# Optimization experiments

Measured on AMD Instinct MI355X. Metric: run time of the kernel, lower is better.

Reference implementation:

```python
import jax, jax.numpy as jnp
import numpy as np

NHEAD, D_K, D_V, D_MODEL = 16, 64, 64, 1024
B, LQ, LK = 2, 2048, 2048
LN_EPS = 1e-6


def setup_inputs() -> dict:
    key = jax.random.key(0)
    ks = jax.random.split(key, 12)
    s = 0.02
    return {
        "q": jax.random.normal(ks[0], (B, LQ, D_MODEL), jnp.float32),
        "k": jax.random.normal(ks[1], (B, LK, D_MODEL), jnp.float32),
        "v": jax.random.normal(ks[2], (B, LK, D_MODEL), jnp.float32),
        "mask": jax.random.randint(ks[3], (B, LQ, LK), 0, 2, jnp.int32),
        "mean": jax.random.uniform(ks[4], (B, LK), jnp.float32, 0.5, 1.5),
        "std": jax.random.uniform(ks[5], (B, LK), jnp.float32, -0.5, 0.5),
        "w_qs": jax.random.normal(ks[6], (D_MODEL, NHEAD * D_K), jnp.float32) * s,
        "w_ks": jax.random.normal(ks[7], (D_MODEL, NHEAD * D_K), jnp.float32) * s,
        "w_vs": jax.random.normal(ks[8], (D_MODEL, NHEAD * D_V), jnp.float32) * s,
        "w_fc": jax.random.normal(ks[9], (NHEAD * D_V, D_MODEL), jnp.float32) * s,
        "ln_gamma": jnp.ones((D_MODEL,), jnp.float32),
        "ln_beta": jnp.zeros((D_MODEL,), jnp.float32),
    }


def _layer_norm(x, gamma, beta):
    mu = jnp.mean(x, axis=-1, keepdims=True)
    var = jnp.mean(jnp.square(x - mu), axis=-1, keepdims=True)
    return (x - mu) * jax.lax.rsqrt(var + LN_EPS) * gamma + beta


def reference(q, k, v, mask, mean, std, w_qs, w_ks, w_vs, w_fc, ln_gamma, ln_beta):
    residual = q
    # projections -> [B, H, L, d]
    qh = (q @ w_qs).reshape(B, LQ, NHEAD, D_K).transpose(0, 2, 1, 3)
    kh = (k @ w_ks).reshape(B, LK, NHEAD, D_K).transpose(0, 2, 1, 3)
    vh = (v @ w_vs).reshape(B, LK, NHEAD, D_V).transpose(0, 2, 1, 3)
    # scores with affine modification: (QK^T * mean + std) / sqrt(d_k)
    attn = jnp.einsum("bhqd,bhkd->bhqk", qh, kh)
    attn = (attn * mean[:, None, None, :] + std[:, None, None, :]) / jnp.sqrt(jnp.float32(D_K))
    attn = jnp.where(mask[:, None, :, :] == 0, jnp.float32(-1e9), attn)
    attn = jax.nn.softmax(attn, axis=-1)
    out = jnp.einsum("bhqk,bhkd->bhqd", attn, vh)  # [B,H,Lq,Dv]
    out = out.transpose(0, 2, 1, 3).reshape(B, LQ, NHEAD * D_V)
    out = out @ w_fc + residual
    return _layer_norm(out, ln_gamma, ln_beta)
```

## Files before the change

kernel.cpp:

```cpp
#include <hip/hip_runtime.h>
#include <math.h>

#define NHEAD 16
#define DK 64
#define DMODEL 1024
#define BB 2
#define LQ 2048
#define LK 2048
#define MROWS (BB * LQ)

typedef __attribute__((ext_vector_type(8))) short short8v;
typedef __attribute__((ext_vector_type(4))) float f32x4;
typedef __attribute__((ext_vector_type(16))) float f32x16;

__device__ __forceinline__ ushort f2bf(float x) {
  uint u = __builtin_bit_cast(uint, x);
  u += 0x7FFFu + ((u >> 16) & 1u);
  return (ushort)(u >> 16);
}
__device__ __forceinline__ float bf2f(ushort h) {
  return __builtin_bit_cast(float, ((uint)h) << 16);
}

__global__ __launch_bounds__(256) void conv_x(const float* __restrict__ x,
                                              ushort* __restrict__ hi,
                                              ushort* __restrict__ lo, int n4) {
  for (int i = blockIdx.x * blockDim.x + threadIdx.x; i < n4;
       i += gridDim.x * blockDim.x) {
    float4 v = ((const float4*)x)[i];
    ushort4 h, l;
    h.x = f2bf(v.x); l.x = f2bf(v.x - bf2f(h.x));
    h.y = f2bf(v.y); l.y = f2bf(v.y - bf2f(h.y));
    h.z = f2bf(v.z); l.z = f2bf(v.z - bf2f(h.z));
    h.w = f2bf(v.w); l.w = f2bf(v.w - bf2f(h.w));
    ((ushort4*)hi)[i] = h;
    ((ushort4*)lo)[i] = l;
  }
}

__global__ __launch_bounds__(256) void conv_wT(
    const float* __restrict__ w0, const float* __restrict__ w1,
    const float* __restrict__ w2, const float* __restrict__ w3,
    ushort* __restrict__ hiB, ushort* __restrict__ loB) {
  const float* W = blockIdx.z == 0 ? w0
                   : blockIdx.z == 1 ? w1
                   : blockIdx.z == 2 ? w2 : w3;
  ushort* hi = hiB + (size_t)blockIdx.z * DMODEL * DMODEL;
  ushort* lo = loB + (size_t)blockIdx.z * DMODEL * DMODEL;
  __shared__ ushort Th[64][66], Tl[64][66];
  const int t = threadIdx.x;
  const int n0 = blockIdx.x * 64, k0 = blockIdx.y * 64;
  const int r = t >> 4, c4 = (t & 15) << 2;
#pragma unroll
  for (int p = 0; p < 4; ++p) {
    const int kr = r + p * 16;
    float4 v = *(const float4*)&W[(size_t)(k0 + kr) * DMODEL + n0 + c4];
    ushort h;
    h = f2bf(v.x); Th[c4 + 0][kr] = h; Tl[c4 + 0][kr] = f2bf(v.x - bf2f(h));
    h = f2bf(v.y); Th[c4 + 1][kr] = h; Tl[c4 + 1][kr] = f2bf(v.y - bf2f(h));
    h = f2bf(v.z); Th[c4 + 2][kr] = h; Tl[c4 + 2][kr] = f2bf(v.z - bf2f(h));
    h = f2bf(v.w); Th[c4 + 3][kr] = h; Tl[c4 + 3][kr] = f2bf(v.w - bf2f(h));
  }
  __syncthreads();
  const int n = t >> 2, g = t & 3;
  uint uh[8], ul[8];
#pragma unroll
  for (int j = 0; j < 8; ++j) {
    uh[j] = *(const uint*)&Th[n][g * 16 + 2 * j];
    ul[j] = *(const uint*)&Tl[n][g * 16 + 2 * j];
  }
  const size_t ob = (size_t)(n0 + n) * DMODEL + k0 + g * 16;
  *(uint4*)&hi[ob] = make_uint4(uh[0], uh[1], uh[2], uh[3]);
  *(uint4*)&hi[ob + 8] = make_uint4(uh[4], uh[5], uh[6], uh[7]);
  *(uint4*)&lo[ob] = make_uint4(ul[0], ul[1], ul[2], ul[3]);
  *(uint4*)&lo[ob + 8] = make_uint4(ul[4], ul[5], ul[6], ul[7]);
}

template <int MODE>
__global__ __launch_bounds__(256, 2) void gemm_mfma(
    const ushort* __restrict__ Ah, const ushort* __restrict__ Al,
    const ushort* __restrict__ Bh, const ushort* __restrict__ Bl,
    ushort* __restrict__ Oh, ushort* __restrict__ Ol,
    float* __restrict__ outF, const float* __restrict__ res) {
  __shared__ __align__(16) ushort As_hi[128 * 32], As_lo[128 * 32];
  __shared__ __align__(16) ushort Bs_hi[128 * 32], Bs_lo[128 * 32];

  const int t = threadIdx.x;
  const int ln = t & 63, wv = t >> 6;
  const int wm = wv >> 1, wn = wv & 1;
  const int n0 = blockIdx.x * 128, m0 = blockIdx.y * 128;

  const int am = t & 127, akg = t >> 7;
  const int bn = am, bkg = akg;

  const ushort* Aph = Ah + (size_t)(m0 + am) * 1024 + akg * 16;
  const ushort* Apl = Al + (size_t)(m0 + am) * 1024 + akg * 16;
  const ushort* Bph = Bh + (size_t)(n0 + bn) * 1024 + bkg * 16;
  const ushort* Bpl = Bl + (size_t)(n0 + bn) * 1024 + bkg * 16;

  short8v ah0 = *(const short8v*)(Aph), ah1 = *(const short8v*)(Aph + 8);
  short8v al0 = *(const short8v*)(Apl), al1 = *(const short8v*)(Apl + 8);
  short8v bh0 = *(const short8v*)(Bph), bh1 = *(const short8v*)(Bph + 8);
  short8v bl0 = *(const short8v*)(Bpl), bl1 = *(const short8v*)(Bpl + 8);

  f32x4 acc[4][4];
#pragma unroll
  for (int i = 0; i < 4; ++i)
#pragma unroll
    for (int j = 0; j < 4; ++j)
#pragma unroll
      for (int r = 0; r < 4; ++r) acc[i][j][r] = 0.f;

  const int swa = (am >> 1) & 3;
  const int s0 = (akg * 2) ^ swa, s1 = (akg * 2 + 1) ^ swa;

  for (int k0 = 0; k0 < 1024; k0 += 32) {
    __syncthreads();
    *(short8v*)&As_hi[am * 32 + s0 * 8] = ah0;
    *(short8v*)&As_hi[am * 32 + s1 * 8] = ah1;
    *(short8v*)&As_lo[am * 32 + s0 * 8] = al0;
    *(short8v*)&As_lo[am * 32 + s1 * 8] = al1;
    *(short8v*)&Bs_hi[bn * 32 + s0 * 8] = bh0;
    *(short8v*)&Bs_hi[bn * 32 + s1 * 8] = bh1;
    *(short8v*)&Bs_lo[bn * 32 + s0 * 8] = bl0;
    *(short8v*)&Bs_lo[bn * 32 + s1 * 8] = bl1;
    __syncthreads();

    if (k0 + 32 < 1024) {
      ah0 = *(const short8v*)(Aph + k0 + 32);
      ah1 = *(const short8v*)(Aph + k0 + 40);
      al0 = *(const short8v*)(Apl + k0 + 32);
      al1 = *(const short8v*)(Apl + k0 + 40);
      bh0 = *(const short8v*)(Bph + k0 + 32);
      bh1 = *(const short8v*)(Bph + k0 + 40);
      bl0 = *(const short8v*)(Bpl + k0 + 32);
      bl1 = *(const short8v*)(Bpl + k0 + 40);
    }

    short8v fah[4], fal[4], fbh[4], fbl[4];
#pragma unroll
    for (int mf = 0; mf < 4; ++mf) {
      const int mr = wm * 64 + mf * 16 + (ln & 15);
      const int sl = (ln >> 4) ^ ((mr >> 1) & 3);
      fah[mf] = *(const short8v*)&As_hi[mr * 32 + sl * 8];
      fal[mf] = *(const short8v*)&As_lo[mr * 32 + sl * 8];
    }
#pragma unroll
    for (int nf = 0; nf < 4; ++nf) {
      const int nr = wn * 64 + nf * 16 + (ln & 15);
      const int sl = (ln >> 4) ^ ((nr >> 1) & 3);
      fbh[nf] = *(const short8v*)&Bs_hi[nr * 32 + sl * 8];
      fbl[nf] = *(const short8v*)&Bs_lo[nr * 32 + sl * 8];
    }
#pragma unroll
    for (int mi = 0; mi < 4; ++mi)
#pragma unroll
      for (int ni = 0; ni < 4; ++ni) {
        acc[mi][ni] = __builtin_amdgcn_mfma_f32_16x16x32_bf16(
            fah[mi], fbh[ni], acc[mi][ni], 0, 0, 0);
        acc[mi][ni] = __builtin_amdgcn_mfma_f32_16x16x32_bf16(
            fal[mi], fbh[ni], acc[mi][ni], 0, 0, 0);
        acc[mi][ni] = __builtin_amdgcn_mfma_f32_16x16x32_bf16(
            fah[mi], fbl[ni], acc[mi][ni], 0, 0, 0);
      }
  }

#pragma unroll
  for (int mi = 0; mi < 4; ++mi)
#pragma unroll
    for (int ni = 0; ni < 4; ++ni) {
      const int ng = n0 + wn * 64 + ni * 16 + (ln & 15);
#pragma unroll
      for (int r = 0; r < 4; ++r) {
        const int mg = m0 + wm * 64 + mi * 16 + (ln >> 4) * 4 + r;
        const float val = acc[mi][ni][r];
        if (MODE == 1) {
          outF[(size_t)mg * 1024 + ng] = val + res[(size_t)mg * 1024 + ng];
        } else {
          const int h = ng >> 6, d = ng & 63;
          const int bb = mg >> 11, l = mg & (LQ - 1);
          size_t idx;
          if (MODE == 0) idx = ((size_t)(bb * NHEAD + h) * LQ + l) * 64 + d;
          else           idx = ((size_t)(bb * NHEAD + h) * 64 + d) * LK + l;
          const ushort hb = f2bf(val);
          Oh[idx] = hb;
          Ol[idx] = f2bf(val - bf2f(hb));
        }
      }
    }
}

__global__ __launch_bounds__(256, 2) void attn_mfma(
    const ushort* __restrict__ Qhh, const ushort* __restrict__ Qhl,
    const ushort* __restrict__ Khh, const ushort* __restrict__ Khl,
    const ushort* __restrict__ VTh, const ushort* __restrict__ VTl,
    const int* __restrict__ mask, const float* __restrict__ mean,
    const float* __restrict__ stdv, ushort* __restrict__ AOh,
    ushort* __restrict__ AOl) {
  __shared__ __align__(16) ushort Ks_hi[32 * 64], Ks_lo[32 * 64];
  __shared__ __align__(16) ushort VT_hi[64 * 40], VT_lo[64 * 40];
  __shared__ __align__(16) ushort P_hi[4][32 * 40], P_lo[4][32 * 40];
  __shared__ float sc_lds[4][32];

  const int t = threadIdx.x;
  const int w = t >> 6, ln = t & 63;
  const int lq = ln & 31;
  const int hi5 = ln >> 5;

  const int q0 = blockIdx.x * 128 + w * 32;
  const int h = blockIdx.y, b = blockIdx.z;

  const size_t hb_ = (size_t)(b * NHEAD + h);
  const ushort* Qh_ = Qhh + hb_ * LQ * 64;
  const ushort* Ql_ = Qhl + hb_ * LQ * 64;
  const ushort* Kh_ = Khh + hb_ * LK * 64;
  const ushort* Kl_ = Khl + hb_ * LK * 64;
  const ushort* Vh_ = VTh + hb_ * 64 * LK;
  const ushort* Vl_ = VTl + hb_ * 64 * LK;

  short8v qf_h[4], qf_l[4];
#pragma unroll
  for (int ds = 0; ds < 4; ++ds) {
    const size_t off = (size_t)(q0 + lq) * 64 + ds * 16 + hi5 * 8;
    qf_h[ds] = *(const short8v*)&Qh_[off];
    qf_l[ds] = *(const short8v*)&Ql_[off];
  }

  const int skr = t >> 3, sds = t & 7;
  const int vd = t >> 2, vg = t & 3;
  const int kslot = sds ^ (skr & 7);

  short8v kp_h = *(const short8v*)&Kh_[(size_t)skr * 64 + sds * 8];
  short8v kp_l = *(const short8v*)&Kl_[(size_t)skr * 64 + sds * 8];
  short8v vp_h = *(const short8v*)&Vh_[(size_t)vd * LK + vg * 8];
  short8v vp_l = *(const short8v*)&Vl_[(size_t)vd * LK + vg * 8];

  f32x16 Oa[2];
#pragma unroll
  for (int dt = 0; dt < 2; ++dt)
#pragma unroll
    for (int r = 0; r < 16; ++r) Oa[dt][r] = 0.f;
  float mrun = -INFINITY, lrun = 0.f;

  for (int k0 = 0; k0 < LK; k0 += 32) {
    __syncthreads();
    *(short8v*)&Ks_hi[skr * 64 + kslot * 8] = kp_h;
    *(short8v*)&Ks_lo[skr * 64 + kslot * 8] = kp_l;
    *(short8v*)&VT_hi[vd * 40 + vg * 8] = vp_h;
    *(short8v*)&VT_lo[vd * 40 + vg * 8] = vp_l;
    __syncthreads();

    float4 mn[4], sd[4];
    int4 mk[4];
#pragma unroll
    for (int g = 0; g < 4; ++g) {
      const int kb = k0 + 8 * g + 4 * hi5;
      mn[g] = *(const float4*)&mean[(size_t)b * LK + kb];
      sd[g] = *(const float4*)&stdv[(size_t)b * LK + kb];
      mk[g] = *(const int4*)&mask[((size_t)b * LQ + q0 + lq) * LK + kb];
    }

    if (k0 + 32 < LK) {
      kp_h = *(const short8v*)&Kh_[(size_t)(k0 + 32 + skr) * 64 + sds * 8];
      kp_l = *(const short8v*)&Kl_[(size_t)(k0 + 32 + skr) * 64 + sds * 8];
      vp_h = *(const short8v*)&Vh_[(size_t)vd * LK + k0 + 32 + vg * 8];
      vp_l = *(const short8v*)&Vl_[(size_t)vd * LK + k0 + 32 + vg * 8];
    }

    f32x16 S;
#pragma unroll
    for (int r = 0; r < 16; ++r) S[r] = 0.f;
#pragma unroll
    for (int ds = 0; ds < 4; ++ds) {
      const int dsl = (ds * 2 + hi5) ^ (lq & 7);
      short8v kf_h = *(const short8v*)&Ks_hi[lq * 64 + dsl * 8];
      short8v kf_l = *(const short8v*)&Ks_lo[lq * 64 + dsl * 8];
      S = __builtin_amdgcn_mfma_f32_32x32x16_bf16(kf_h, qf_h[ds], S, 0, 0, 0);
      S = __builtin_amdgcn_mfma_f32_32x32x16_bf16(kf_l, qf_h[ds], S, 0, 0, 0);
      S = __builtin_amdgcn_mfma_f32_32x32x16_bf16(kf_h, qf_l[ds], S, 0, 0, 0);
    }

    float p[16];
    float tmax = -INFINITY;
#pragma unroll
    for (int r = 0; r < 16; ++r) {
      const int g = r >> 2, j = r & 3;
      float v = fmaf(S[r], ((const float*)&mn[g])[j] * 0.125f,
                     ((const float*)&sd[g])[j] * 0.125f);
      v = (((const int*)&mk[g])[j] == 0) ? -1e9f : v;
      p[r] = v;
      tmax = fmaxf(tmax, v);
    }
    tmax = fmaxf(tmax, __shfl_xor(tmax, 32, 64));
    const float mnew = fmaxf(mrun, tmax);
    const float scl = __expf(mrun - mnew);
    float psum = 0.f;
#pragma unroll
    for (int r = 0; r < 16; ++r) {
      p[r] = __expf(p[r] - mnew);
      psum += p[r];
    }
    psum += __shfl_xor(psum, 32, 64);
    lrun = lrun * scl + psum;
    mrun = mnew;

#pragma unroll
    for (int r = 0; r < 16; r += 2) {
      const int k = (r & 3) + 8 * (r >> 2) + 4 * hi5;
      ushort h0 = f2bf(p[r]), h1 = f2bf(p[r + 1]);
      *(uint*)&P_hi[w][lq * 40 + k] = (uint)h0 | ((uint)h1 << 16);
      ushort l0 = f2bf(p[r] - bf2f(h0)), l1 = f2bf(p[r + 1] - bf2f(h1));
      *(uint*)&P_lo[w][lq * 40 + k] = (uint)l0 | ((uint)l1 << 16);
    }
    sc_lds[w][lq] = scl;

    float4 s4[4];
#pragma unroll
    for (int g = 0; g < 4; ++g)
      s4[g] = *(const float4*)&sc_lds[w][8 * g + 4 * hi5];
#pragma unroll
    for (int dt = 0; dt < 2; ++dt)
#pragma unroll
      for (int r = 0; r < 16; ++r) Oa[dt][r] *= ((const float*)&s4[r >> 2])[r & 3];

#pragma unroll
    for (int dt = 0; dt < 2; ++dt)
#pragma unroll
      for (int ki = 0; ki < 2; ++ki) {
        short8v pah = *(const short8v*)&P_hi[w][lq * 40 + ki * 16 + hi5 * 8];
        short8v pal = *(const short8v*)&P_lo[w][lq * 40 + ki * 16 + hi5 * 8];
        short8v vbh =
            *(const short8v*)&VT_hi[(dt * 32 + lq) * 40 + ki * 16 + hi5 * 8];
        short8v vbl =
            *(const short8v*)&VT_lo[(dt * 32 + lq) * 40 + ki * 16 + hi5 * 8];
        Oa[dt] = __builtin_amdgcn_mfma_f32_32x32x16_bf16(pah, vbh, Oa[dt], 0, 0, 0);
        Oa[dt] = __builtin_amdgcn_mfma_f32_32x32x16_bf16(pal, vbh, Oa[dt], 0, 0, 0);
        Oa[dt] = __builtin_amdgcn_mfma_f32_32x32x16_bf16(pah, vbl, Oa[dt], 0, 0, 0);
      }
  }

  sc_lds[w][lq] = 1.0f / lrun;
  float4 iv[4];
#pragma unroll
  for (int g = 0; g < 4; ++g)
    iv[g] = *(const float4*)&sc_lds[w][8 * g + 4 * hi5];
#pragma unroll
  for (int dt = 0; dt < 2; ++dt)
#pragma unroll
    for (int r = 0; r < 16; ++r) {
      const int ql = (r & 3) + 8 * (r >> 2) + 4 * hi5;
      const float v = Oa[dt][r] * ((const float*)&iv[r >> 2])[r & 3];
      const size_t idx =
          (size_t)(b * LQ + q0 + ql) * DMODEL + h * 64 + dt * 32 + lq;
      const ushort hbv = f2bf(v);
      AOh[idx] = hbv;
      AOl[idx] = f2bf(v - bf2f(hbv));
    }
}

__global__ __launch_bounds__(256) void ln_kernel(float* __restrict__ io,
                                                 const float* __restrict__ gamma,
                                                 const float* __restrict__ beta) {
  const int row = blockIdx.x;
  const int t = threadIdx.x;
  float* base = io + (size_t)row * DMODEL;
  float4 x = *(const float4*)&base[t << 2];
  float s = x.x + x.y + x.z + x.w;
#pragma unroll
  for (int xm = 1; xm < 64; xm <<= 1) s += __shfl_xor(s, xm, 64);
  __shared__ float part[4];
  __shared__ float smu, svar;
  if ((t & 63) == 0) part[t >> 6] = s;
  __syncthreads();
  if (t == 0) smu = (part[0] + part[1] + part[2] + part[3]) * (1.0f / DMODEL);
  __syncthreads();
  const float mu = smu;
  const float d0 = x.x - mu, d1 = x.y - mu, d2 = x.z - mu, d3 = x.w - mu;
  float s2 = d0 * d0 + d1 * d1 + d2 * d2 + d3 * d3;
#pragma unroll
  for (int xm = 1; xm < 64; xm <<= 1) s2 += __shfl_xor(s2, xm, 64);
  if ((t & 63) == 0) part[t >> 6] = s2;
  __syncthreads();
  if (t == 0) svar = (part[0] + part[1] + part[2] + part[3]) * (1.0f / DMODEL);
  __syncthreads();
  const float inv = rsqrtf(svar + 1e-6f);
  float4 g = *(const float4*)&gamma[t << 2];
  float4 be = *(const float4*)&beta[t << 2];
  float4 o;
  o.x = d0 * inv * g.x + be.x;
  o.y = d1 * inv * g.y + be.y;
  o.z = d2 * inv * g.z + be.z;
  o.w = d3 * inv * g.w + be.w;
  *(float4*)&base[t << 2] = o;
}

extern "C" void kernel_launch(void* const* d_in, const int* in_sizes, int n_in,
                              void* d_out, int out_size, void* d_ws,
                              size_t ws_size, hipStream_t stream) {
  const float* q = (const float*)d_in[0];
  const float* k = (const float*)d_in[1];
  const float* v = (const float*)d_in[2];
  const int* mask = (const int*)d_in[3];
  const float* mean = (const float*)d_in[4];
  const float* stdv = (const float*)d_in[5];
  const float* w_qs = (const float*)d_in[6];
  const float* w_ks = (const float*)d_in[7];
  const float* w_vs = (const float*)d_in[8];
  const float* w_fc = (const float*)d_in[9];
  const float* gamma = (const float*)d_in[10];
  const float* beta = (const float*)d_in[11];
  float* out = (float*)d_out;

  const size_t PL = (size_t)MROWS * DMODEL;
  const size_t WL = (size_t)DMODEL * DMODEL;
  ushort* wsp = (ushort*)d_ws;
  ushort* qh_h = wsp;
  ushort* qh_l = qh_h + PL;
  ushort* kh_h = qh_l + PL;
  ushort* kh_l = kh_h + PL;
  ushort* vt_h = kh_l + PL;
  ushort* vt_l = vt_h + PL;
  ushort* wT_h = vt_l + PL;
  ushort* wT_l = wT_h + 4 * WL;
  ushort* xs_h = wT_l + 4 * WL;
  ushort* xs_l = xs_h + PL;
  ushort* ao_h = xs_h;
  ushort* ao_l = xs_l;

  dim3 blk(256);
  dim3 gg(DMODEL / 128, MROWS / 128);
  const int n4 = MROWS * DMODEL / 4;

  conv_wT<<<dim3(16, 16, 4), blk, 0, stream>>>(w_qs, w_ks, w_vs, w_fc, wT_h, wT_l);

  conv_x<<<2048, blk, 0, stream>>>(q, xs_h, xs_l, n4);
  gemm_mfma<0><<<gg, blk, 0, stream>>>(xs_h, xs_l, wT_h + 0 * WL, wT_l + 0 * WL,
                                       qh_h, qh_l, nullptr, nullptr);
  conv_x<<<2048, blk, 0, stream>>>(k, xs_h, xs_l, n4);
  gemm_mfma<0><<<gg, blk, 0, stream>>>(xs_h, xs_l, wT_h + 1 * WL, wT_l + 1 * WL,
                                       kh_h, kh_l, nullptr, nullptr);
  conv_x<<<2048, blk, 0, stream>>>(v, xs_h, xs_l, n4);
  gemm_mfma<2><<<gg, blk, 0, stream>>>(xs_h, xs_l, wT_h + 2 * WL, wT_l + 2 * WL,
                                       vt_h, vt_l, nullptr, nullptr);

  attn_mfma<<<dim3(LQ / 128, NHEAD, BB), blk, 0, stream>>>(
      qh_h, qh_l, kh_h, kh_l, vt_h, vt_l, mask, mean, stdv, ao_h, ao_l);

  gemm_mfma<1><<<gg, blk, 0, stream>>>(ao_h, ao_l, wT_h + 3 * WL, wT_l + 3 * WL,
                                       nullptr, nullptr, out, q);
  ln_kernel<<<MROWS, blk, 0, stream>>>(out, gamma, beta);
}
```

Before: 547.4 us.

## Batch QKV conversion and projections, keep P in registers, skip rescale

The three input conversions and the three projection GEMMs each become a single launch, with blockIdx.z selecting Q, K or V and picking the output layout. In attention, the softmax probabilities are converted to bf16 hi/lo parts and rearranged with v_permlane32_swap, so they feed the PV MFMAs straight from registers instead of going through an LDS round trip. The online-softmax rescale of the accumulator is skipped when no lane's running max increases. This removes launch overhead and LDS traffic and gives more parallelism per launch, at the cost of a larger workspace and inline asm that only works on this architecture.

```diff
diff --git a/kernel.cpp b/kernel.cpp
--- a/kernel.cpp
+++ b/kernel.cpp
@@ -8,10 +8,13 @@
 #define LQ 2048
 #define LK 2048
 #define MROWS (BB * LQ)
+#define PLANE ((size_t)MROWS * DMODEL)
+#define WPLANE ((size_t)DMODEL * DMODEL)
 
 typedef __attribute__((ext_vector_type(8))) short short8v;
 typedef __attribute__((ext_vector_type(4))) float f32x4;
 typedef __attribute__((ext_vector_type(16))) float f32x16;
+typedef __attribute__((ext_vector_type(4))) uint uint4v;
 
 __device__ __forceinline__ ushort f2bf(float x) {
   uint u = __builtin_bit_cast(uint, x);
@@ -22,17 +25,22 @@
   return __builtin_bit_cast(float, ((uint)h) << 16);
 }
 
-__global__ __launch_bounds__(256) void conv_x(const float* __restrict__ x,
-                                              ushort* __restrict__ hi,
-                                              ushort* __restrict__ lo, int n4) {
+__global__ __launch_bounds__(256) void conv_x3(
+    const float* __restrict__ q, const float* __restrict__ k,
+    const float* __restrict__ v, ushort* __restrict__ hiB,
+    ushort* __restrict__ loB, int n4) {
+  const int z = blockIdx.z;
+  const float* x = z == 0 ? q : z == 1 ? k : v;
+  ushort* hi = hiB + (size_t)z * PLANE;
+  ushort* lo = loB + (size_t)z * PLANE;
   for (int i = blockIdx.x * blockDim.x + threadIdx.x; i < n4;
        i += gridDim.x * blockDim.x) {
-    float4 v = ((const float4*)x)[i];
+    float4 vv = ((const float4*)x)[i];
     ushort4 h, l;
-    h.x = f2bf(v.x); l.x = f2bf(v.x - bf2f(h.x));
-    h.y = f2bf(v.y); l.y = f2bf(v.y - bf2f(h.y));
-    h.z = f2bf(v.z); l.z = f2bf(v.z - bf2f(h.z));
-    h.w = f2bf(v.w); l.w = f2bf(v.w - bf2f(h.w));
+    h.x = f2bf(vv.x); l.x = f2bf(vv.x - bf2f(h.x));
+    h.y = f2bf(vv.y); l.y = f2bf(vv.y - bf2f(h.y));
+    h.z = f2bf(vv.z); l.z = f2bf(vv.z - bf2f(h.z));
+    h.w = f2bf(vv.w); l.w = f2bf(vv.w - bf2f(h.w));
     ((ushort4*)hi)[i] = h;
     ((ushort4*)lo)[i] = l;
   }
@@ -45,8 +53,8 @@
   const float* W = blockIdx.z == 0 ? w0
                    : blockIdx.z == 1 ? w1
                    : blockIdx.z == 2 ? w2 : w3;
-  ushort* hi = hiB + (size_t)blockIdx.z * DMODEL * DMODEL;
-  ushort* lo = loB + (size_t)blockIdx.z * DMODEL * DMODEL;
+  ushort* hi = hiB + (size_t)blockIdx.z * WPLANE;
+  ushort* lo = loB + (size_t)blockIdx.z * WPLANE;
   __shared__ ushort Th[64][66], Tl[64][66];
   const int t = threadIdx.x;
   const int n0 = blockIdx.x * 64, k0 = blockIdx.y * 64;
@@ -89,6 +97,13 @@
   const int ln = t & 63, wv = t >> 6;
   const int wm = wv >> 1, wn = wv & 1;
   const int n0 = blockIdx.x * 128, m0 = blockIdx.y * 128;
+  const int zz = blockIdx.z;
+
+  if (MODE == 3) {
+    Ah += (size_t)zz * PLANE;  Al += (size_t)zz * PLANE;
+    Bh += (size_t)zz * WPLANE; Bl += (size_t)zz * WPLANE;
+    Oh += (size_t)zz * PLANE;  Ol += (size_t)zz * PLANE;
+  }
 
   const int am = t & 127, akg = t >> 7;
   const int bn = am, bkg = akg;
@@ -180,8 +195,8 @@
           const int h = ng >> 6, d = ng & 63;
           const int bb = mg >> 11, l = mg & (LQ - 1);
           size_t idx;
-          if (MODE == 0) idx = ((size_t)(bb * NHEAD + h) * LQ + l) * 64 + d;
-          else           idx = ((size_t)(bb * NHEAD + h) * 64 + d) * LK + l;
+          if (zz == 2) idx = ((size_t)(bb * NHEAD + h) * 64 + d) * LK + l;
+          else         idx = ((size_t)(bb * NHEAD + h) * LQ + l) * 64 + d;
           const ushort hb = f2bf(val);
           Oh[idx] = hb;
           Ol[idx] = f2bf(val - bf2f(hb));
@@ -199,7 +214,6 @@
     ushort* __restrict__ AOl) {
   __shared__ __align__(16) ushort Ks_hi[32 * 64], Ks_lo[32 * 64];
   __shared__ __align__(16) ushort VT_hi[64 * 40], VT_lo[64 * 40];
-  __shared__ __align__(16) ushort P_hi[4][32 * 40], P_lo[4][32 * 40];
   __shared__ float sc_lds[4][32];
 
   const int t = threadIdx.x;
@@ -292,8 +306,8 @@
       tmax = fmaxf(tmax, v);
     }
     tmax = fmaxf(tmax, __shfl_xor(tmax, 32, 64));
-    const float mnew = fmaxf(mrun, tmax);
-    const float scl = __expf(mrun - mnew);
+    const bool need = __any(tmax > mrun);
+    const float mnew = need ? fmaxf(mrun, tmax) : mrun;
     float psum = 0.f;
 #pragma unroll
     for (int r = 0; r < 16; ++r) {
@@ -301,41 +315,69 @@
       psum += p[r];
     }
     psum += __shfl_xor(psum, 32, 64);
-    lrun = lrun * scl + psum;
-    mrun = mnew;
-
-#pragma unroll
-    for (int r = 0; r < 16; r += 2) {
-      const int k = (r & 3) + 8 * (r >> 2) + 4 * hi5;
-      ushort h0 = f2bf(p[r]), h1 = f2bf(p[r + 1]);
-      *(uint*)&P_hi[w][lq * 40 + k] = (uint)h0 | ((uint)h1 << 16);
-      ushort l0 = f2bf(p[r] - bf2f(h0)), l1 = f2bf(p[r + 1] - bf2f(h1));
-      *(uint*)&P_lo[w][lq * 40 + k] = (uint)l0 | ((uint)l1 << 16);
-    }
-    sc_lds[w][lq] = scl;
-
-    float4 s4[4];
-#pragma unroll
-    for (int g = 0; g < 4; ++g)
-      s4[g] = *(const float4*)&sc_lds[w][8 * g + 4 * hi5];
+    if (need) {
+      const float scl = __expf(mrun - mnew);
+      lrun = lrun * scl + psum;
+      mrun = mnew;
+      sc_lds[w][lq] = scl;
+      float4 s4[4];
+#pragma unroll
+      for (int g = 0; g < 4; ++g)
+        s4[g] = *(const float4*)&sc_lds[w][8 * g + 4 * hi5];
+#pragma unroll
+      for (int dt = 0; dt < 2; ++dt)
+#pragma unroll
+        for (int r = 0; r < 16; ++r)
+          Oa[dt][r] *= ((const float*)&s4[r >> 2])[r & 3];
+    } else {
+      lrun += psum;
+    }
+
+    uint ch[8], cl[8];
+#pragma unroll
+    for (int j = 0; j < 8; ++j) {
+      const float a = p[2 * j], c = p[2 * j + 1];
+      const ushort h0 = __builtin_bit_cast(ushort, (__bf16)a);
+      const ushort h1 = __builtin_bit_cast(ushort, (__bf16)c);
+      ch[j] = (uint)h0 | ((uint)h1 << 16);
+      const float l0 = a - bf2f(h0);
+      const float l1 = c - bf2f(h1);
+      const ushort g0 = __builtin_bit_cast(ushort, (__bf16)l0);
+      const ushort g1 = __builtin_bit_cast(ushort, (__bf16)l1);
+      cl[j] = (uint)g0 | ((uint)g1 << 16);
+    }
+    asm("v_permlane32_swap_b32 %0, %1" : "+v"(ch[0]), "+v"(ch[2]));
+    asm("v_permlane32_swap_b32 %0, %1" : "+v"(ch[1]), "+v"(ch[3]));
+    asm("v_permlane32_swap_b32 %0, %1" : "+v"(ch[4]), "+v"(ch[6]));
+    asm("v_permlane32_swap_b32 %0, %1" : "+v"(ch[5]), "+v"(ch[7]));
+    asm("v_permlane32_swap_b32 %0, %1" : "+v"(cl[0]), "+v"(cl[2]));
+    asm("v_permlane32_swap_b32 %0, %1" : "+v"(cl[1]), "+v"(cl[3]));
+    asm("v_permlane32_swap_b32 %0, %1" : "+v"(cl[4]), "+v"(cl[6]));
+    asm("v_permlane32_swap_b32 %0, %1" : "+v"(cl[5]), "+v"(cl[7]));
+    short8v paH[2], paL[2];
+    {
+      uint4v u;
+      u = (uint4v){ch[0], ch[1], ch[2], ch[3]};
+      paH[0] = __builtin_bit_cast(short8v, u);
+      u = (uint4v){ch[4], ch[5], ch[6], ch[7]};
+      paH[1] = __builtin_bit_cast(short8v, u);
+      u = (uint4v){cl[0], cl[1], cl[2], cl[3]};
+      paL[0] = __builtin_bit_cast(short8v, u);
+      u = (uint4v){cl[4], cl[5], cl[6], cl[7]};
+      paL[1] = __builtin_bit_cast(short8v, u);
+    }
+
 #pragma unroll
     for (int dt = 0; dt < 2; ++dt)
 #pragma unroll
-      for (int r = 0; r < 16; ++r) Oa[dt][r] *= ((const float*)&s4[r >> 2])[r & 3];
-
-#pragma unroll
-    for (int dt = 0; dt < 2; ++dt)
-#pragma unroll
       for (int ki = 0; ki < 2; ++ki) {
-        short8v pah = *(const short8v*)&P_hi[w][lq * 40 + ki * 16 + hi5 * 8];
-        short8v pal = *(const short8v*)&P_lo[w][lq * 40 + ki * 16 + hi5 * 8];
         short8v vbh =
             *(const short8v*)&VT_hi[(dt * 32 + lq) * 40 + ki * 16 + hi5 * 8];
         short8v vbl =
             *(const short8v*)&VT_lo[(dt * 32 + lq) * 40 + ki * 16 + hi5 * 8];
-        Oa[dt] = __builtin_amdgcn_mfma_f32_32x32x16_bf16(pah, vbh, Oa[dt], 0, 0, 0);
-        Oa[dt] = __builtin_amdgcn_mfma_f32_32x32x16_bf16(pal, vbh, Oa[dt], 0, 0, 0);
-        Oa[dt] = __builtin_amdgcn_mfma_f32_32x32x16_bf16(pah, vbl, Oa[dt], 0, 0, 0);
+        Oa[dt] = __builtin_amdgcn_mfma_f32_32x32x16_bf16(paH[ki], vbh, Oa[dt], 0, 0, 0);
+        Oa[dt] = __builtin_amdgcn_mfma_f32_32x32x16_bf16(paL[ki], vbh, Oa[dt], 0, 0, 0);
+        Oa[dt] = __builtin_amdgcn_mfma_f32_32x32x16_bf16(paH[ki], vbl, Oa[dt], 0, 0, 0);
       }
   }
 
@@ -411,42 +453,29 @@
   const float* beta = (const float*)d_in[11];
   float* out = (float*)d_out;
 
-  const size_t PL = (size_t)MROWS * DMODEL;
-  const size_t WL = (size_t)DMODEL * DMODEL;
-  ushort* wsp = (ushort*)d_ws;
-  ushort* qh_h = wsp;
-  ushort* qh_l = qh_h + PL;
-  ushort* kh_h = qh_l + PL;
-  ushort* kh_l = kh_h + PL;
-  ushort* vt_h = kh_l + PL;
-  ushort* vt_l = vt_h + PL;
-  ushort* wT_h = vt_l + PL;
-  ushort* wT_l = wT_h + 4 * WL;
-  ushort* xs_h = wT_l + 4 * WL;
-  ushort* xs_l = xs_h + PL;
-  ushort* ao_h = xs_h;
-  ushort* ao_l = xs_l;
+  ushort* xinH = (ushort*)d_ws;
+  ushort* xinL = xinH + 3 * PLANE;
+  ushort* prH  = xinL + 3 * PLANE;
+  ushort* prL  = prH + 3 * PLANE;
+  ushort* wT_h = prL + 3 * PLANE;
+  ushort* wT_l = wT_h + 4 * WPLANE;
+  ushort* aoH = xinH;
+  ushort* aoL = xinL;
 
   dim3 blk(256);
-  dim3 gg(DMODEL / 128, MROWS / 128);
   const int n4 = MROWS * DMODEL / 4;
 
   conv_wT<<<dim3(16, 16, 4), blk, 0, stream>>>(w_qs, w_ks, w_vs, w_fc, wT_h, wT_l);
-
-  conv_x<<<2048, blk, 0, stream>>>(q, xs_h, xs_l, n4);
-  gemm_mfma<0><<<gg, blk, 0, stream>>>(xs_h, xs_l, wT_h + 0 * WL, wT_l + 0 * WL,
-                                       qh_h, qh_l, nullptr, nullptr);
-  conv_x<<<2048, blk, 0, stream>>>(k, xs_h, xs_l, n4);
-  gemm_mfma<0><<<gg, blk, 0, stream>>>(xs_h, xs_l, wT_h + 1 * WL, wT_l + 1 * WL,
-                                       kh_h, kh_l, nullptr, nullptr);
-  conv_x<<<2048, blk, 0, stream>>>(v, xs_h, xs_l, n4);
-  gemm_mfma<2><<<gg, blk, 0, stream>>>(xs_h, xs_l, wT_h + 2 * WL, wT_l + 2 * WL,
-                                       vt_h, vt_l, nullptr, nullptr);
-
-  attn_mfma<<<dim3(LQ / 128, NHEAD, BB), blk, 0, stream>>>(
-      qh_h, qh_l, kh_h, kh_l, vt_h, vt_l, mask, mean, stdv, ao_h, ao_l);
-
-  gemm_mfma<1><<<gg, blk, 0, stream>>>(ao_h, ao_l, wT_h + 3 * WL, wT_l + 3 * WL,
-                                       nullptr, nullptr, out, q);
+  conv_x3<<<dim3(512, 1, 3), blk, 0, stream>>>(q, k, v, xinH, xinL, n4);
+
+  gemm_mfma<3><<<dim3(8, 32, 3), blk, 0, stream>>>(
+      xinH, xinL, wT_h, wT_l, prH, prL, nullptr, nullptr);
+
+  attn_mfma<<<dim3(16, 16, 2), blk, 0, stream>>>(
+      prH, prL, prH + PLANE, prL + PLANE, prH + 2 * PLANE, prL + 2 * PLANE,
+      mask, mean, stdv, aoH, aoL);
+
+  gemm_mfma<1><<<dim3(8, 32), blk, 0, stream>>>(
+      aoH, aoL, wT_h + 3 * WPLANE, wT_l + 3 * WPLANE, nullptr, nullptr, out, q);
   ln_kernel<<<MROWS, blk, 0, stream>>>(out, gamma, beta);
 }
```

Result: faster. 519.5 us (-5.1%).
